# Kernel optimization log

Hardware: AMD Instinct MI355X
Metric: run time of the kernel (lower is better)

Reference implementation:

```python
import math
import jax, jax.numpy as jnp
import numpy as np

VOCAB, EMB, H, NL = 100, 128, 384, 4
B, L = 32, 1024
CTX_IN = 3 * 100


def _glorot(key, shape):
    fan = shape[-1]
    return jax.random.normal(key, shape, dtype=jnp.float32) / np.sqrt(fan)


def setup_inputs() -> dict:
    key = jax.random.key(0)
    ks = jax.random.split(key, 16)
    x = jax.random.randint(ks[0], (B, L), 0, VOCAB)
    context = jax.random.normal(ks[1], (B, L, 3, 100), dtype=jnp.float32)
    h = jnp.zeros((NL, B, H), dtype=jnp.float32)
    c = jnp.zeros((NL, B, H), dtype=jnp.float32)
    emb = _glorot(ks[2], (VOCAB, EMB)).at[71].set(0.0)  # padding_idx=71
    ctx_W = _glorot(ks[3], (EMB, CTX_IN))
    ctx_b = jnp.zeros((EMB,), jnp.float32)
    Wih0 = _glorot(ks[4], (4 * H, 2 * EMB))            # layer 0 input = emb||ctx
    Wih_rest = _glorot(ks[5], (NL - 1, 4 * H, H))
    Whh = _glorot(ks[6], (NL, 4 * H, H))
    bih = jnp.zeros((NL, 4 * H), jnp.float32)
    bhh = jnp.zeros((NL, 4 * H), jnp.float32)
    Wa = _glorot(ks[7], (H, H))
    comb_W = _glorot(ks[8], (H, 2 * H))
    comb_b = jnp.zeros((H,), jnp.float32)
    fc_W = _glorot(ks[9], (VOCAB, H))
    fc_b = jnp.zeros((VOCAB,), jnp.float32)
    return dict(x=x, context=context, h=h, c=c, emb=emb, ctx_W=ctx_W, ctx_b=ctx_b,
                Wih0=Wih0, Wih_rest=Wih_rest, Whh=Whh, bih=bih, bhh=bhh,
                Wa=Wa, comb_W=comb_W, comb_b=comb_b, fc_W=fc_W, fc_b=fc_b)


def _lstm_layer(x, h0, c0, Wih, Whh, bih, bhh):
    # x: [B,L,D] -> scan over time
    def step(carry, xt):
        h, c = carry
        g = xt @ Wih.T + h @ Whh.T + bih + bhh  # [B,4H]
        i, f, gg, o = jnp.split(g, 4, axis=-1)  # torch gate order i,f,g,o
        c = jax.nn.sigmoid(f) * c + jax.nn.sigmoid(i) * jnp.tanh(gg)
        h = jax.nn.sigmoid(o) * jnp.tanh(c)
        return (h, c), h
    (hf, cf), ys = jax.lax.scan(step, (h0, c0), jnp.swapaxes(x, 0, 1))
    return jnp.swapaxes(ys, 0, 1), hf, cf


def _forward(x, context, h, c, emb, ctx_W, ctx_b, Wih0, Wih_rest, Whh, bih, bhh,
             Wa, comb_W, comb_b, fc_W, fc_b):
    x_embed = emb[x]                                        # [B,L,EMB]
    ctx_flat = context.reshape(context.shape[0], context.shape[1], -1)
    ctx_proj = ctx_flat @ ctx_W.T + ctx_b                   # [B,L,EMB]
    inp = jnp.concatenate([x_embed, ctx_proj], axis=-1)     # [B,L,2*EMB]
    hs, cs = [], []
    for l in range(NL):
        Wih = Wih0 if l == 0 else Wih_rest[l - 1]
        inp, hf, cf = _lstm_layer(inp, h[l], c[l], Wih, Whh[l], bih[l], bhh[l])
        hs.append(hf); cs.append(cf)
    out = inp                                               # [B,L,H]
    keys = out @ Wa.T
    scores = jnp.einsum('bqd,bkd->bqk', out, keys) / math.sqrt(H)
    Lq = out.shape[1]
    mask = jnp.tril(jnp.ones((Lq, Lq), dtype=bool))
    scores = jnp.where(mask[None], scores, jnp.float32(-1e30))
    attn = jax.nn.softmax(scores, axis=-1)
    ctx_vec = jnp.einsum('bqk,bkd->bqd', attn, out)
    combined = jnp.tanh(jnp.concatenate([out, ctx_vec], axis=-1) @ comb_W.T + comb_b)
    logits = combined @ fc_W.T + fc_b
    return logits, jnp.stack(hs), jnp.stack(cs)


def reference(x, context, h, c, emb, ctx_W, ctx_b, Wih0, Wih_rest, Whh, bih, bhh,
              Wa, comb_W, comb_b, fc_W, fc_b):
    return _forward(x, context, h, c, emb, ctx_W, ctx_b, Wih0, Wih_rest, Whh,
                    bih, bhh, Wa, comb_W, comb_b, fc_W, fc_b)
```

## Files before the change

kernel.cpp:

```cpp
#include <hip/hip_runtime.h>

typedef unsigned int  uint32;
typedef unsigned long long u64;
typedef unsigned short bf16u;
typedef __attribute__((ext_vector_type(8))) short s8v;
typedef __attribute__((ext_vector_type(4))) float f4v;
typedef __attribute__((ext_vector_type(16))) float f16v;

#define PL   6144
#define PL64 3072
#define PAR  12288
#define HB2  24576

__device__ __forceinline__ float fast_tanh(float x) {
    x = fminf(9.f, fmaxf(-9.f, x));
    float e = __expf(2.f * x);
    return (e - 1.f) / (e + 1.f);
}
__device__ __forceinline__ float sigmoidf(float x) {
    return 1.f / (1.f + __expf(-x));
}
__device__ __forceinline__ bf16u f2bf(float f) {
    uint32 u = __float_as_uint(f);
    u += 0x7fffu + ((u >> 16) & 1u);
    return (bf16u)(u >> 16);
}
__device__ __forceinline__ float bf2f(bf16u u) {
    return __uint_as_float(((uint32)u) << 16);
}
__device__ __forceinline__ uint32 pack2bf(float lo, float hi) {
    return (uint32)f2bf(lo) | ((uint32)f2bf(hi) << 16);
}
__device__ __forceinline__ float bflo(uint32 p) { return __uint_as_float(p << 16); }
__device__ __forceinline__ float bfhi(uint32 p) { return __uint_as_float(p & 0xffff0000u); }

__device__ __forceinline__ s8v ldfrag(const u64* p) {
    union { u64 q[2]; s8v v; } u;
    u.q[0] = __hip_atomic_load(p,     __ATOMIC_RELAXED, __HIP_MEMORY_SCOPE_AGENT);
    u.q[1] = __hip_atomic_load(p + 1, __ATOMIC_RELAXED, __HIP_MEMORY_SCOPE_AGENT);
    return u.v;
}

__global__ void __launch_bounds__(128) embed_ctx_kernel(
    const int* __restrict__ x, const float* __restrict__ ctx,
    const float* __restrict__ emb, const float* __restrict__ ctxW,
    const float* __restrict__ ctxb, bf16u* __restrict__ inp)
{
    const int r0 = blockIdx.x * 16;
    const int tid = threadIdx.x;
    __shared__ float cs[16][301];
    __shared__ int xs[16];
    for (int i = tid; i < 16 * 300; i += 128) {
        int row = i / 300, k = i - row * 300;
        int rt = r0 + row, b = rt & 31, t = rt >> 5;
        cs[row][k] = ctx[((size_t)b * 1024 + t) * 300 + k];
    }
    if (tid < 16) {
        int rt = r0 + tid;
        xs[tid] = x[(rt & 31) * 1024 + (rt >> 5)];
    }
    __syncthreads();
    float acc[16];
    #pragma unroll
    for (int row = 0; row < 16; ++row) acc[row] = 0.f;
    for (int k = 0; k < 300; ++k) {
        float w = ctxW[tid * 300 + k];
        #pragma unroll
        for (int row = 0; row < 16; ++row) acc[row] = fmaf(w, cs[row][k], acc[row]);
    }
    float bb = ctxb[tid];
    for (int row = 0; row < 16; ++row) {
        size_t base = (size_t)(r0 + row) * 256;
        inp[base + tid]       = f2bf(emb[xs[row] * 128 + tid]);
        inp[base + 128 + tid] = f2bf(acc[row] + bb);
    }
}

__global__ void __launch_bounds__(256) gemm_kernel(
    const bf16u* __restrict__ A0, const bf16u* __restrict__ A1, int K0,
    const float* __restrict__ W, const float* __restrict__ bias1,
    void* __restrict__ Cout, int M, int N, int K, int mode)
{
    __shared__ bf16u As[128][40];
    __shared__ bf16u Whi[64][40];
    __shared__ bf16u Wlo[64][40];
    const int tid = threadIdx.x;
    const int bn = blockIdx.x * 64, bm = blockIdx.y * 128;
    const int wave = tid >> 6, lane = tid & 63;
    const int ncol = lane & 15, quad = lane >> 4;
    const int lr = tid >> 2, lk = (tid & 3) * 8;

    f4v acc[2][4];
    #pragma unroll
    for (int i = 0; i < 2; ++i)
        #pragma unroll
        for (int j = 0; j < 4; ++j) acc[i][j] = (f4v){0.f, 0.f, 0.f, 0.f};

    const int wrow = bn + lr;
    for (int k0 = 0; k0 < K; k0 += 32) {
        const bf16u* Ab; int kb, lda;
        if (k0 < K0) { Ab = A0; kb = k0; lda = K0; }
        else         { Ab = A1; kb = k0 - K0; lda = K - K0; }
        uint4 av0 = *(const uint4*)(Ab + (size_t)(bm + lr) * lda + kb + lk);
        uint4 av1 = *(const uint4*)(Ab + (size_t)(bm + 64 + lr) * lda + kb + lk);
        float4 w0 = make_float4(0.f, 0.f, 0.f, 0.f), w1 = w0;
        if (wrow < N) {
            const float* wp = W + (size_t)wrow * K + k0 + lk;
            w0 = *(const float4*)wp;
            w1 = *(const float4*)(wp + 4);
        }
        __syncthreads();
        *(uint4*)&As[lr][lk] = av0;
        *(uint4*)&As[64 + lr][lk] = av1;
        {
            bf16u h[8], l[8];
            float wf[8] = {w0.x, w0.y, w0.z, w0.w, w1.x, w1.y, w1.z, w1.w};
            #pragma unroll
            for (int j = 0; j < 8; ++j) {
                h[j] = f2bf(wf[j]);
                l[j] = f2bf(wf[j] - bf2f(h[j]));
            }
            #pragma unroll
            for (int j = 0; j < 8; ++j) Whi[lr][lk + j] = h[j];
            #pragma unroll
            for (int j = 0; j < 8; ++j) Wlo[lr][lk + j] = l[j];
        }
        __syncthreads();
        s8v aF[2], bH[4], bL[4];
        #pragma unroll
        for (int mt = 0; mt < 2; ++mt)
            aF[mt] = *(const s8v*)&As[wave * 32 + mt * 16 + ncol][quad * 8];
        #pragma unroll
        for (int nt = 0; nt < 4; ++nt) {
            bH[nt] = *(const s8v*)&Whi[nt * 16 + ncol][quad * 8];
            bL[nt] = *(const s8v*)&Wlo[nt * 16 + ncol][quad * 8];
        }
        #pragma unroll
        for (int mt = 0; mt < 2; ++mt)
            #pragma unroll
            for (int nt = 0; nt < 4; ++nt) {
                acc[mt][nt] = __builtin_amdgcn_mfma_f32_16x16x32_bf16(
                    aF[mt], bH[nt], acc[mt][nt], 0, 0, 0);
                acc[mt][nt] = __builtin_amdgcn_mfma_f32_16x16x32_bf16(
                    aF[mt], bL[nt], acc[mt][nt], 0, 0, 0);
            }
    }

    #pragma unroll
    for (int nt = 0; nt < 4; ++nt) {
        const int col = bn + nt * 16 + ncol;
        if (col >= N) continue;
        float bb = bias1 ? bias1[col] : 0.f;
        #pragma unroll
        for (int mt = 0; mt < 2; ++mt) {
            const int rowb = bm + wave * 32 + mt * 16 + quad * 4;
            if (mode == 3) {
                #pragma unroll
                for (int r = 0; r < 4; ++r) {
                    int row = rowb + r;
                    int b = row & 31, t = row >> 5;
                    ((float*)Cout)[((size_t)b * 1024 + t) * (size_t)N + col] =
                        acc[mt][nt][r] + bb;
                }
            } else {
                #pragma unroll
                for (int r = 0; r < 4; ++r) {
                    float v = acc[mt][nt][r] + bb;
                    if (mode == 2) v = fast_tanh(v);
                    ((bf16u*)Cout)[(size_t)(rowb + r) * N + col] = f2bf(v);
                }
            }
        }
    }
}

__device__ __forceinline__ void scoped_barrier(uint32* flags, uint32 r,
                                               int tid, int l, int bid) {
    __syncthreads();
    if (tid == 0)
        __hip_atomic_store(&flags[bid * 32], r, __ATOMIC_RELAXED, __HIP_MEMORY_SCOPE_AGENT);
    const int lo = (l > 0) ? (l - 1) * 48 : 0;
    const int nf = ((l > 0) + 1 + (l < 3)) * 48;
    if (tid < nf) {
        while (__hip_atomic_load(&flags[(lo + tid) * 32], __ATOMIC_RELAXED,
                                 __HIP_MEMORY_SCOPE_AGENT) < r)
            __builtin_amdgcn_s_sleep(1);
    }
    __syncthreads();
}

__global__ void __launch_bounds__(256, 1) lstm_wave_kernel(
    const bf16u* __restrict__ inp,
    const float* __restrict__ Wih0,
    const float* __restrict__ WihR,
    const float* __restrict__ Whh,
    const float* __restrict__ bih, const float* __restrict__ bhh,
    const float* __restrict__ h_in, const float* __restrict__ c_in,
    uint32* __restrict__ y3bm,
    uint32* __restrict__ hbuf,
    uint32* __restrict__ flags,
    float* __restrict__ hs_out, float* __restrict__ cs_out)
{
    extern __shared__ char sm[];
    const int tid = threadIdx.x, bid = blockIdx.x;
    const int l = bid / 48, sub = bid - l * 48;
    const int j0 = sub * 8;
    const int wave = tid >> 6, lane = tid & 63;
    const int row32 = lane & 31;
    const int khalf = lane >> 5;
    const int n = row32;

    const int Kx = l ? 384 : 256;
    const int WSTR = l ? 392 : 264;
    const int wbytes = 2 * 32 * WSTR * 2;
    bf16u* wlds  = (bf16u*)sm;
    float* gates = (float*)(sm + wbytes);

    const float* WhhL = Whh + (size_t)l * 1536 * 384;
    const float* WihL = l ? (WihR + (size_t)(l - 1) * 1536 * 384) : Wih0;
    const float* bihL = bih + l * 1536;
    const float* bhhL = bhh + l * 1536;
    uint32* hbL = hbuf + (size_t)l * HB2;
    uint32* ybL = l ? (hbuf + (size_t)(l - 1) * HB2) : nullptr;

    const int h0c = wave * 6;
    const int x0c = wave * 4;

    s8v Bh6[6], Bl6[6];
    {
        const int wrow = (n >> 3) * 384 + j0 + (n & 7);
        #pragma unroll
        for (int i = 0; i < 6; ++i) {
            const float* wp = WhhL + (size_t)wrow * 384 + (h0c + i) * 16 + khalf * 8;
            s8v hi, lo;
            #pragma unroll
            for (int j = 0; j < 8; ++j) {
                float w = wp[j];
                bf16u wh = f2bf(w);
                bf16u wl = f2bf(w - bf2f(wh));
                hi[j] = (short)wh; lo[j] = (short)wl;
            }
            Bh6[i] = hi; Bl6[i] = lo;
        }
    }
    for (int r2 = 0; r2 < 32; ++r2) {
        int rg = (r2 >> 3) * 384 + j0 + (r2 & 7);
        for (int k = tid; k < Kx; k += 256) {
            float w = WihL[(size_t)rg * Kx + k];
            bf16u wh = f2bf(w);
            wlds[r2 * WSTR + k] = wh;
            wlds[32 * WSTR + r2 * WSTR + k] = f2bf(w - bf2f(wh));
        }
    }

    const int ub = tid & 31, jp = tid >> 5;
    const int jg0 = j0 + 2 * jp;
    const int wbase = (sub * 32 + ub) * 4 + jp;
    float c0r = 0.f, c1r = 0.f, h0l = 0.f, h1l = 0.f;
    float bI0 = 0, bF0 = 0, bG0 = 0, bO0 = 0, bI1 = 0, bF1 = 0, bG1 = 0, bO1 = 0;

    if (tid < 128) {
        bI0 = bihL[jg0] + bhhL[jg0];
        bF0 = bihL[384 + jg0] + bhhL[384 + jg0];
        bG0 = bihL[768 + jg0] + bhhL[768 + jg0];
        bO0 = bihL[1152 + jg0] + bhhL[1152 + jg0];
        bI1 = bihL[jg0 + 1] + bhhL[jg0 + 1];
        bF1 = bihL[384 + jg0 + 1] + bhhL[384 + jg0 + 1];
        bG1 = bihL[768 + jg0 + 1] + bhhL[768 + jg0 + 1];
        bO1 = bihL[1152 + jg0 + 1] + bhhL[1152 + jg0 + 1];
        float ha = h_in[(size_t)l * 12288 + ub * 384 + jg0];
        float hb = h_in[(size_t)l * 12288 + ub * 384 + jg0 + 1];
        bf16u ha_h = f2bf(ha); bf16u ha_l = f2bf(ha - bf2f(ha_h));
        bf16u hb_h = f2bf(hb); bf16u hb_l = f2bf(hb - bf2f(hb_h));
        __hip_atomic_store(&hbL[wbase],
                           (uint32)ha_h | ((uint32)hb_h << 16),
                           __ATOMIC_RELAXED, __HIP_MEMORY_SCOPE_AGENT);
        __hip_atomic_store(&hbL[PL + wbase],
                           (uint32)ha_l | ((uint32)hb_l << 16),
                           __ATOMIC_RELAXED, __HIP_MEMORY_SCOPE_AGENT);
        c0r = c_in[(size_t)l * 12288 + ub * 384 + jg0];
        c1r = c_in[(size_t)l * 12288 + ub * 384 + jg0 + 1];
    }
    scoped_barrier(flags, 1u, tid, l, bid);

    for (int r = 0; r < 1027; ++r) {
        const int t = r - l;
        if ((unsigned)t < 1024u) {
            const u64* hB = (const u64*)(hbL + (t & 1) * PAR);
            uint32* hW = hbL + ((t + 1) & 1) * PAR;

            f16v cHH = {0.f,0.f,0.f,0.f,0.f,0.f,0.f,0.f,
                        0.f,0.f,0.f,0.f,0.f,0.f,0.f,0.f};
            f16v cLH = cHH, cHL = cHH;

            s8v Ah[6], Al[6];
            #pragma unroll
            for (int i = 0; i < 6; ++i) {
                const int co = (((h0c + i) * 2 + khalf) * 32 + row32) * 2;
                Ah[i] = ldfrag(hB + co);
                Al[i] = ldfrag(hB + PL64 + co);
            }

            if (l) {
                const u64* yB = (const u64*)(ybL + ((t + 1) & 1) * PAR);
                s8v Ayh[6], Ayl[6];
                #pragma unroll
                for (int i = 0; i < 6; ++i) {
                    const int co = (((h0c + i) * 2 + khalf) * 32 + row32) * 2;
                    Ayh[i] = ldfrag(yB + co);
                    Ayl[i] = ldfrag(yB + PL64 + co);
                }
                #pragma unroll
                for (int i = 0; i < 6; ++i) {
                    cHH = __builtin_amdgcn_mfma_f32_32x32x16_bf16(Ah[i], Bh6[i], cHH, 0, 0, 0);
                    cLH = __builtin_amdgcn_mfma_f32_32x32x16_bf16(Al[i], Bh6[i], cLH, 0, 0, 0);
                    cHL = __builtin_amdgcn_mfma_f32_32x32x16_bf16(Ah[i], Bl6[i], cHL, 0, 0, 0);
                }
                #pragma unroll
                for (int i = 0; i < 6; ++i) {
                    const int kt = h0c + i;
                    s8v Bxh = *(const s8v*)&wlds[n * 392 + kt * 16 + khalf * 8];
                    s8v Bxl = *(const s8v*)&wlds[32 * 392 + n * 392 + kt * 16 + khalf * 8];
                    cHH = __builtin_amdgcn_mfma_f32_32x32x16_bf16(Ayh[i], Bxh, cHH, 0, 0, 0);
                    cLH = __builtin_amdgcn_mfma_f32_32x32x16_bf16(Ayl[i], Bxh, cLH, 0, 0, 0);
                    cHL = __builtin_amdgcn_mfma_f32_32x32x16_bf16(Ayh[i], Bxl, cHL, 0, 0, 0);
                }
            } else {
                const uint4* irow = (const uint4*)(inp + ((size_t)t * 32 + row32) * 256);
                s8v Ai[4];
                #pragma unroll
                for (int i = 0; i < 4; ++i) {
                    union { uint4 u; s8v v; } cv;
                    cv.u = irow[(x0c + i) * 2 + khalf];
                    Ai[i] = cv.v;
                }
                #pragma unroll
                for (int i = 0; i < 6; ++i) {
                    cHH = __builtin_amdgcn_mfma_f32_32x32x16_bf16(Ah[i], Bh6[i], cHH, 0, 0, 0);
                    cLH = __builtin_amdgcn_mfma_f32_32x32x16_bf16(Al[i], Bh6[i], cLH, 0, 0, 0);
                    cHL = __builtin_amdgcn_mfma_f32_32x32x16_bf16(Ah[i], Bl6[i], cHL, 0, 0, 0);
                }
                #pragma unroll
                for (int i = 0; i < 4; ++i) {
                    const int kt = x0c + i;
                    s8v Bxh = *(const s8v*)&wlds[n * 264 + kt * 16 + khalf * 8];
                    s8v Bxl = *(const s8v*)&wlds[32 * 264 + n * 264 + kt * 16 + khalf * 8];
                    cHH = __builtin_amdgcn_mfma_f32_32x32x16_bf16(Ai[i], Bxh, cHH, 0, 0, 0);
                    cHL = __builtin_amdgcn_mfma_f32_32x32x16_bf16(Ai[i], Bxl, cHL, 0, 0, 0);
                }
            }
            {
                float* ps = gates + wave * 1056;
                #pragma unroll
                for (int reg = 0; reg < 16; ++reg) {
                    const int brow = (reg & 3) + 8 * (reg >> 2) + 4 * khalf;
                    ps[n * 33 + brow] = cHH[reg] + cLH[reg] + cHL[reg];
                }
            }
            __syncthreads();

            if (tid < 128) {
                const int jj0 = 2 * jp, jj1 = 2 * jp + 1;
                #define GS(g) (gates[(g) * 33 + ub] + gates[1056 + (g) * 33 + ub] + \
                               gates[2112 + (g) * 33 + ub] + gates[3168 + (g) * 33 + ub])
                float pi0 = GS(jj0)      + bI0;
                float pf0 = GS(8 + jj0)  + bF0;
                float pg0 = GS(16 + jj0) + bG0;
                float po0 = GS(24 + jj0) + bO0;
                float pi1 = GS(jj1)      + bI1;
                float pf1 = GS(8 + jj1)  + bF1;
                float pg1 = GS(16 + jj1) + bG1;
                float po1 = GS(24 + jj1) + bO1;
                #undef GS
                c0r = sigmoidf(pf0) * c0r + sigmoidf(pi0) * fast_tanh(pg0);
                c1r = sigmoidf(pf1) * c1r + sigmoidf(pi1) * fast_tanh(pg1);
                float hv0 = sigmoidf(po0) * fast_tanh(c0r);
                float hv1 = sigmoidf(po1) * fast_tanh(c1r);
                h0l = hv0; h1l = hv1;
                bf16u h0h = f2bf(hv0); bf16u h0lo = f2bf(hv0 - bf2f(h0h));
                bf16u h1h = f2bf(hv1); bf16u h1lo = f2bf(hv1 - bf2f(h1h));
                uint32 hiw = (uint32)h0h | ((uint32)h1h << 16);
                uint32 low = (uint32)h0lo | ((uint32)h1lo << 16);
                __hip_atomic_store(&hW[wbase], hiw,
                                   __ATOMIC_RELAXED, __HIP_MEMORY_SCOPE_AGENT);
                __hip_atomic_store(&hW[PL + wbase], low,
                                   __ATOMIC_RELAXED, __HIP_MEMORY_SCOPE_AGENT);
                if (l == 3)
                    y3bm[(size_t)t * 6144 + wbase] = hiw;
            }
        }
        scoped_barrier(flags, (uint32)(r + 2), tid, l, bid);
    }

    if (tid < 128) {
        hs_out[(size_t)l * 12288 + ub * 384 + jg0]     = h0l;
        hs_out[(size_t)l * 12288 + ub * 384 + jg0 + 1] = h1l;
        cs_out[(size_t)l * 12288 + ub * 384 + jg0]     = c0r;
        cs_out[(size_t)l * 12288 + ub * 384 + jg0 + 1] = c1r;
    }
}

__global__ void __launch_bounds__(256) transpose_y_kernel(
    const uint32* __restrict__ in, uint32* __restrict__ out)
{
    const int t = blockIdx.x;
    const int tid = threadIdx.x;
    __shared__ uint32 lds[32 * 197];
    const uint32* src = in + (size_t)t * 6144;
    #pragma unroll
    for (int k = 0; k < 24; ++k) {
        int i = k * 256 + tid;
        int sub = i >> 7, b = (i >> 2) & 31, q = i & 3;
        lds[b * 197 + sub * 4 + q] = src[i];
    }
    __syncthreads();
    uint32* dst = out + (size_t)t * 32 * 192;
    #pragma unroll
    for (int k = 0; k < 24; ++k) {
        int i = k * 256 + tid;
        int b = i / 192, c = i - b * 192;
        dst[b * 192 + c] = lds[b * 197 + c];
    }
}

__global__ void __launch_bounds__(256, 1) attn_kernel(
    const bf16u* __restrict__ outy, const bf16u* __restrict__ keys,
    bf16u* __restrict__ ctxv)
{
    extern __shared__ char smem[];
    uint32* Qs  = (uint32*)smem;
    uint32* Ks  = (uint32*)(smem + 26112);
    bf16u*  Vt  = (bf16u*)(smem + 52224);
    float*  Ss  = (float*)(smem + 95232);
    bf16u*  Ph  = (bf16u*)(smem + 112128);
    bf16u*  Pl  = (bf16u*)(smem + 115200);
    float*  m_s = (float*)(smem + 118272);
    float*  l_s = m_s + 32;
    float*  al_s = m_s + 64;

    const int b = blockIdx.y;
    const int q0 = blockIdx.x * 32;
    const int tid = threadIdx.x;
    const int wave = tid >> 6, lane = tid & 63;
    const int lrow = lane & 31, lhalf = lane >> 5;

    for (int i = tid; i < 32 * 192; i += 256) {
        int q = i / 192, dp = i - q * 192;
        Qs[q * 204 + dp] = ((const uint32*)outy)[((size_t)(q0 + q) * 32 + b) * 192 + dp];
    }
    if (tid < 32) { m_s[tid] = -3e38f; l_s[tid] = 0.f; }

    f16v O[3];
    #pragma unroll
    for (int g = 0; g < 3; ++g)
        #pragma unroll
        for (int r = 0; r < 16; ++r) O[g][r] = 0.f;

    const int nkt = blockIdx.x + 1;
    for (int kt = 0; kt < nkt; ++kt) {
        const int k0 = kt * 32;
        __syncthreads();
        for (int i = tid; i < 32 * 192; i += 256) {
            int kk = i / 192, dp = i - kk * 192;
            size_t rb = ((size_t)(k0 + kk) * 32 + b) * 192;
            Ks[kk * 204 + dp] = ((const uint32*)keys)[rb + dp];
            uint32 vv = ((const uint32*)outy)[rb + dp];
            Vt[(2 * dp) * 56 + kk]     = (bf16u)(vv & 0xffffu);
            Vt[(2 * dp + 1) * 56 + kk] = (bf16u)(vv >> 16);
        }
        __syncthreads();

        {
            f16v s;
            #pragma unroll
            for (int r = 0; r < 16; ++r) s[r] = 0.f;
            #pragma unroll
            for (int i6 = 0; i6 < 6; ++i6) {
                const int kc = wave * 6 + i6;
                s8v a  = *(const s8v*)((const bf16u*)Qs + lrow * 408 + kc * 16 + lhalf * 8);
                s8v kb = *(const s8v*)((const bf16u*)Ks + lrow * 408 + kc * 16 + lhalf * 8);
                s = __builtin_amdgcn_mfma_f32_32x32x16_bf16(a, kb, s, 0, 0, 0);
            }
            float* ps = Ss + wave * 1056;
            #pragma unroll
            for (int r = 0; r < 16; ++r) {
                const int q = (r & 3) + 8 * (r >> 2) + 4 * lhalf;
                ps[q * 33 + lrow] = s[r];
            }
        }
        __syncthreads();

        if (tid < 32) {
            const int q = tid;
            float sv[32];
            float mt = m_s[q];
            #pragma unroll
            for (int k = 0; k < 32; ++k) {
                float s = Ss[q * 33 + k] + Ss[1056 + q * 33 + k]
                        + Ss[2112 + q * 33 + k] + Ss[3168 + q * 33 + k];
                s *= 0.051031036307982884f;
                sv[k] = ((k0 + k) <= (q0 + q)) ? s : -1e30f;
                mt = fmaxf(mt, sv[k]);
            }
            float alpha = __expf(m_s[q] - mt);
            float l = l_s[q] * alpha;
            #pragma unroll
            for (int k = 0; k < 32; ++k) {
                float pv = __expf(sv[k] - mt);
                l += pv;
                bf16u ph = f2bf(pv);
                Ph[q * 48 + k] = ph;
                Pl[q * 48 + k] = f2bf(pv - bf2f(ph));
            }
            m_s[q] = mt; l_s[q] = l; al_s[q] = alpha;
        }
        __syncthreads();

        {
            float ar[16];
            #pragma unroll
            for (int r = 0; r < 16; ++r)
                ar[r] = al_s[(r & 3) + 8 * (r >> 2) + 4 * lhalf];
            #pragma unroll
            for (int g = 0; g < 3; ++g)
                #pragma unroll
                for (int r = 0; r < 16; ++r) O[g][r] *= ar[r];

            s8v pa0 = *(const s8v*)(Ph + lrow * 48 + lhalf * 8);
            s8v pa1 = *(const s8v*)(Ph + lrow * 48 + 16 + lhalf * 8);
            s8v pl0 = *(const s8v*)(Pl + lrow * 48 + lhalf * 8);
            s8v pl1 = *(const s8v*)(Pl + lrow * 48 + 16 + lhalf * 8);
            #pragma unroll
            for (int g = 0; g < 3; ++g) {
                const int d = (wave * 3 + g) * 32 + lrow;
                s8v v0 = *(const s8v*)(Vt + d * 56 + lhalf * 8);
                s8v v1 = *(const s8v*)(Vt + d * 56 + 16 + lhalf * 8);
                O[g] = __builtin_amdgcn_mfma_f32_32x32x16_bf16(pa0, v0, O[g], 0, 0, 0);
                O[g] = __builtin_amdgcn_mfma_f32_32x32x16_bf16(pl0, v0, O[g], 0, 0, 0);
                O[g] = __builtin_amdgcn_mfma_f32_32x32x16_bf16(pa1, v1, O[g], 0, 0, 0);
                O[g] = __builtin_amdgcn_mfma_f32_32x32x16_bf16(pl1, v1, O[g], 0, 0, 0);
            }
        }
    }

    __syncthreads();
    if (tid < 32) al_s[tid] = 1.f / l_s[tid];
    __syncthreads();
    {
        float ir[16];
        #pragma unroll
        for (int r = 0; r < 16; ++r)
            ir[r] = al_s[(r & 3) + 8 * (r >> 2) + 4 * lhalf];
        bf16u* Os = (bf16u*)Ks;
        #pragma unroll
        for (int g = 0; g < 3; ++g) {
            const int d = (wave * 3 + g) * 32 + lrow;
            #pragma unroll
            for (int r = 0; r < 16; ++r) {
                const int q = (r & 3) + 8 * (r >> 2) + 4 * lhalf;
                Os[q * 408 + d] = f2bf(O[g][r] * ir[r]);
            }
        }
    }
    __syncthreads();
    for (int i = tid; i < 32 * 192; i += 256) {
        int q = i / 192, dp = i - q * 192;
        ((uint32*)ctxv)[((size_t)(q0 + q) * 32 + b) * 192 + dp] = Ks[q * 204 + dp];
    }
}

extern "C" void kernel_launch(void* const* d_in, const int* in_sizes, int n_in,
                              void* d_out, int out_size, void* d_ws, size_t ws_size,
                              hipStream_t stream) {
    (void)in_sizes; (void)n_in; (void)out_size; (void)ws_size;
    const int*   x        = (const int*)d_in[0];
    const float* context  = (const float*)d_in[1];
    const float* h_in     = (const float*)d_in[2];
    const float* c_in     = (const float*)d_in[3];
    const float* emb      = (const float*)d_in[4];
    const float* ctx_W    = (const float*)d_in[5];
    const float* ctx_b    = (const float*)d_in[6];
    const float* Wih0     = (const float*)d_in[7];
    const float* Wih_rest = (const float*)d_in[8];
    const float* Whh      = (const float*)d_in[9];
    const float* bih      = (const float*)d_in[10];
    const float* bhh      = (const float*)d_in[11];
    const float* Wa       = (const float*)d_in[12];
    const float* comb_W   = (const float*)d_in[13];
    const float* comb_b   = (const float*)d_in[14];
    const float* fc_W     = (const float*)d_in[15];
    const float* fc_b     = (const float*)d_in[16];
    float* out = (float*)d_out;

    char* wsb = (char*)d_ws;
    uint32* flags = (uint32*)(wsb + 0);
    uint32* hbuf  = (uint32*)(wsb + 32768);
    uint32* y3bm  = (uint32*)(wsb + 458752);
    bf16u*  y3    = (bf16u*)(wsb + 25624576ull);
    bf16u*  inp   = (bf16u*)(wsb + 50790400ull);
    bf16u*  keysu = (bf16u*)(wsb + 50790400ull);
    bf16u*  ctxvu = (bf16u*)(wsb + 458752);
    bf16u*  combu = (bf16u*)(wsb + 50790400ull);

    hipMemsetAsync(d_ws, 0, 32768, stream);

    static int smem_set = 0;
    if (!smem_set) {
        hipFuncSetAttribute((const void*)lstm_wave_kernel,
                            hipFuncAttributeMaxDynamicSharedMemorySize, 67072);
        hipFuncSetAttribute((const void*)attn_kernel,
                            hipFuncAttributeMaxDynamicSharedMemorySize, 118656);
        smem_set = 1;
    }

    embed_ctx_kernel<<<2048, 128, 0, stream>>>(x, context, emb, ctx_W, ctx_b, inp);

    const size_t HS_OFF = (size_t)32768 * 100;
    lstm_wave_kernel<<<192, 256, 67072, stream>>>(
        inp, Wih0, Wih_rest, Whh, bih, bhh, h_in, c_in,
        y3bm, hbuf, flags, out + HS_OFF, out + HS_OFF + 49152);

    transpose_y_kernel<<<1024, 256, 0, stream>>>(y3bm, (uint32*)y3);

    gemm_kernel<<<dim3(6, 256), 256, 0, stream>>>(
        y3, nullptr, 384, Wa, nullptr, keysu, 32768, 384, 384, 1);
    attn_kernel<<<dim3(32, 32), 256, 118656, stream>>>(y3, keysu, ctxvu);
    gemm_kernel<<<dim3(6, 256), 256, 0, stream>>>(
        y3, ctxvu, 384, comb_W, comb_b, combu, 32768, 384, 768, 2);
    gemm_kernel<<<dim3(2, 256), 256, 0, stream>>>(
        combu, nullptr, 384, fc_W, fc_b, out, 32768, 100, 384, 3);
}
```

Measured before the change: 5.766 ms.

## Halve LSTM wavefront block count by giving each block 16 hidden units

The persistent LSTM kernel now runs 24 blocks per layer (96 total) instead of 48, and each block computes 16 hidden units with two 32-column MFMA tiles. The hidden-state buffer layout, the scoped barrier fan-in, the LDS weight and gate sizes, and the transpose kernel's indexing all change to match. The aim is to cut the per-step cross-block barrier cost (fewer flags to poll, fewer participants) and reuse the A fragments across two B tiles. In exchange each block does twice the MFMA work per step and needs about 134 KB of LDS.

```diff
diff --git a/kernel.cpp b/kernel.cpp
--- a/kernel.cpp
+++ b/kernel.cpp
@@ -179,8 +179,8 @@
     __syncthreads();
     if (tid == 0)
         __hip_atomic_store(&flags[bid * 32], r, __ATOMIC_RELAXED, __HIP_MEMORY_SCOPE_AGENT);
-    const int lo = (l > 0) ? (l - 1) * 48 : 0;
-    const int nf = ((l > 0) + 1 + (l < 3)) * 48;
+    const int lo = (l > 0) ? (l - 1) * 24 : 0;
+    const int nf = ((l > 0) + 1 + (l < 3)) * 24;
     if (tid < nf) {
         while (__hip_atomic_load(&flags[(lo + tid) * 32], __ATOMIC_RELAXED,
                                  __HIP_MEMORY_SCOPE_AGENT) < r)
@@ -203,16 +203,15 @@
 {
     extern __shared__ char sm[];
     const int tid = threadIdx.x, bid = blockIdx.x;
-    const int l = bid / 48, sub = bid - l * 48;
-    const int j0 = sub * 8;
+    const int l = bid / 24, sub = bid - l * 24;
+    const int j0 = sub * 16;
     const int wave = tid >> 6, lane = tid & 63;
     const int row32 = lane & 31;
     const int khalf = lane >> 5;
-    const int n = row32;
 
     const int Kx = l ? 384 : 256;
     const int WSTR = l ? 392 : 264;
-    const int wbytes = 2 * 32 * WSTR * 2;
+    const int wbytes = 2 * 64 * WSTR * 2;
     bf16u* wlds  = (bf16u*)sm;
     float* gates = (float*)(sm + wbytes);
 
@@ -226,9 +225,11 @@
     const int h0c = wave * 6;
     const int x0c = wave * 4;
 
-    s8v Bh6[6], Bl6[6];
-    {
-        const int wrow = (n >> 3) * 384 + j0 + (n & 7);
+    s8v Bh[2][6], Bl[2][6];
+    #pragma unroll
+    for (int nt = 0; nt < 2; ++nt) {
+        const int n = nt * 32 + row32;
+        const int wrow = (n >> 4) * 384 + j0 + (n & 15);
         #pragma unroll
         for (int i = 0; i < 6; ++i) {
             const float* wp = WhhL + (size_t)wrow * 384 + (h0c + i) * 16 + khalf * 8;
@@ -240,34 +241,33 @@
                 bf16u wl = f2bf(w - bf2f(wh));
                 hi[j] = (short)wh; lo[j] = (short)wl;
             }
-            Bh6[i] = hi; Bl6[i] = lo;
-        }
-    }
-    for (int r2 = 0; r2 < 32; ++r2) {
-        int rg = (r2 >> 3) * 384 + j0 + (r2 & 7);
+            Bh[nt][i] = hi; Bl[nt][i] = lo;
+        }
+    }
+    for (int r2 = 0; r2 < 64; ++r2) {
+        int rg = (r2 >> 4) * 384 + j0 + (r2 & 15);
         for (int k = tid; k < Kx; k += 256) {
             float w = WihL[(size_t)rg * Kx + k];
             bf16u wh = f2bf(w);
             wlds[r2 * WSTR + k] = wh;
-            wlds[32 * WSTR + r2 * WSTR + k] = f2bf(w - bf2f(wh));
+            wlds[64 * WSTR + r2 * WSTR + k] = f2bf(w - bf2f(wh));
         }
     }
 
     const int ub = tid & 31, jp = tid >> 5;
     const int jg0 = j0 + 2 * jp;
-    const int wbase = (sub * 32 + ub) * 4 + jp;
+    const int wbase = (sub * 32 + ub) * 8 + jp;
     float c0r = 0.f, c1r = 0.f, h0l = 0.f, h1l = 0.f;
-    float bI0 = 0, bF0 = 0, bG0 = 0, bO0 = 0, bI1 = 0, bF1 = 0, bG1 = 0, bO1 = 0;
-
-    if (tid < 128) {
-        bI0 = bihL[jg0] + bhhL[jg0];
-        bF0 = bihL[384 + jg0] + bhhL[384 + jg0];
-        bG0 = bihL[768 + jg0] + bhhL[768 + jg0];
-        bO0 = bihL[1152 + jg0] + bhhL[1152 + jg0];
-        bI1 = bihL[jg0 + 1] + bhhL[jg0 + 1];
-        bF1 = bihL[384 + jg0 + 1] + bhhL[384 + jg0 + 1];
-        bG1 = bihL[768 + jg0 + 1] + bhhL[768 + jg0 + 1];
-        bO1 = bihL[1152 + jg0 + 1] + bhhL[1152 + jg0 + 1];
+
+    float bI0 = bihL[jg0] + bhhL[jg0];
+    float bF0 = bihL[384 + jg0] + bhhL[384 + jg0];
+    float bG0 = bihL[768 + jg0] + bhhL[768 + jg0];
+    float bO0 = bihL[1152 + jg0] + bhhL[1152 + jg0];
+    float bI1 = bihL[jg0 + 1] + bhhL[jg0 + 1];
+    float bF1 = bihL[384 + jg0 + 1] + bhhL[384 + jg0 + 1];
+    float bG1 = bihL[768 + jg0 + 1] + bhhL[768 + jg0 + 1];
+    float bO1 = bihL[1152 + jg0 + 1] + bhhL[1152 + jg0 + 1];
+    {
         float ha = h_in[(size_t)l * 12288 + ub * 384 + jg0];
         float hb = h_in[(size_t)l * 12288 + ub * 384 + jg0 + 1];
         bf16u ha_h = f2bf(ha); bf16u ha_l = f2bf(ha - bf2f(ha_h));
@@ -289,14 +289,15 @@
             const u64* hB = (const u64*)(hbL + (t & 1) * PAR);
             uint32* hW = hbL + ((t + 1) & 1) * PAR;
 
-            f16v cHH = {0.f,0.f,0.f,0.f,0.f,0.f,0.f,0.f,
-                        0.f,0.f,0.f,0.f,0.f,0.f,0.f,0.f};
-            f16v cLH = cHH, cHL = cHH;
+            f16v c0HH = {0.f,0.f,0.f,0.f,0.f,0.f,0.f,0.f,
+                         0.f,0.f,0.f,0.f,0.f,0.f,0.f,0.f};
+            f16v c0LH = c0HH, c0HL = c0HH;
+            f16v c1HH = c0HH, c1LH = c0HH, c1HL = c0HH;
 
             s8v Ah[6], Al[6];
             #pragma unroll
             for (int i = 0; i < 6; ++i) {
-                const int co = (((h0c + i) * 2 + khalf) * 32 + row32) * 2;
+                const int co = ((h0c + i) * 32 + row32) * 4 + khalf * 2;
                 Ah[i] = ldfrag(hB + co);
                 Al[i] = ldfrag(hB + PL64 + co);
             }
@@ -306,24 +307,32 @@
                 s8v Ayh[6], Ayl[6];
                 #pragma unroll
                 for (int i = 0; i < 6; ++i) {
-                    const int co = (((h0c + i) * 2 + khalf) * 32 + row32) * 2;
+                    const int co = ((h0c + i) * 32 + row32) * 4 + khalf * 2;
                     Ayh[i] = ldfrag(yB + co);
                     Ayl[i] = ldfrag(yB + PL64 + co);
                 }
                 #pragma unroll
                 for (int i = 0; i < 6; ++i) {
-                    cHH = __builtin_amdgcn_mfma_f32_32x32x16_bf16(Ah[i], Bh6[i], cHH, 0, 0, 0);
-                    cLH = __builtin_amdgcn_mfma_f32_32x32x16_bf16(Al[i], Bh6[i], cLH, 0, 0, 0);
-                    cHL = __builtin_amdgcn_mfma_f32_32x32x16_bf16(Ah[i], Bl6[i], cHL, 0, 0, 0);
+                    c0HH = __builtin_amdgcn_mfma_f32_32x32x16_bf16(Ah[i], Bh[0][i], c0HH, 0, 0, 0);
+                    c0LH = __builtin_amdgcn_mfma_f32_32x32x16_bf16(Al[i], Bh[0][i], c0LH, 0, 0, 0);
+                    c0HL = __builtin_amdgcn_mfma_f32_32x32x16_bf16(Ah[i], Bl[0][i], c0HL, 0, 0, 0);
+                    c1HH = __builtin_amdgcn_mfma_f32_32x32x16_bf16(Ah[i], Bh[1][i], c1HH, 0, 0, 0);
+                    c1LH = __builtin_amdgcn_mfma_f32_32x32x16_bf16(Al[i], Bh[1][i], c1LH, 0, 0, 0);
+                    c1HL = __builtin_amdgcn_mfma_f32_32x32x16_bf16(Ah[i], Bl[1][i], c1HL, 0, 0, 0);
                 }
                 #pragma unroll
                 for (int i = 0; i < 6; ++i) {
                     const int kt = h0c + i;
-                    s8v Bxh = *(const s8v*)&wlds[n * 392 + kt * 16 + khalf * 8];
-                    s8v Bxl = *(const s8v*)&wlds[32 * 392 + n * 392 + kt * 16 + khalf * 8];
-                    cHH = __builtin_amdgcn_mfma_f32_32x32x16_bf16(Ayh[i], Bxh, cHH, 0, 0, 0);
-                    cLH = __builtin_amdgcn_mfma_f32_32x32x16_bf16(Ayl[i], Bxh, cLH, 0, 0, 0);
-                    cHL = __builtin_amdgcn_mfma_f32_32x32x16_bf16(Ayh[i], Bxl, cHL, 0, 0, 0);
+                    s8v B0h = *(const s8v*)&wlds[row32 * 392 + kt * 16 + khalf * 8];
+                    s8v B0l = *(const s8v*)&wlds[64 * 392 + row32 * 392 + kt * 16 + khalf * 8];
+                    s8v B1h = *(const s8v*)&wlds[(32 + row32) * 392 + kt * 16 + khalf * 8];
+                    s8v B1l = *(const s8v*)&wlds[64 * 392 + (32 + row32) * 392 + kt * 16 + khalf * 8];
+                    c0HH = __builtin_amdgcn_mfma_f32_32x32x16_bf16(Ayh[i], B0h, c0HH, 0, 0, 0);
+                    c0LH = __builtin_amdgcn_mfma_f32_32x32x16_bf16(Ayl[i], B0h, c0LH, 0, 0, 0);
+                    c0HL = __builtin_amdgcn_mfma_f32_32x32x16_bf16(Ayh[i], B0l, c0HL, 0, 0, 0);
+                    c1HH = __builtin_amdgcn_mfma_f32_32x32x16_bf16(Ayh[i], B1h, c1HH, 0, 0, 0);
+                    c1LH = __builtin_amdgcn_mfma_f32_32x32x16_bf16(Ayl[i], B1h, c1LH, 0, 0, 0);
+                    c1HL = __builtin_amdgcn_mfma_f32_32x32x16_bf16(Ayh[i], B1l, c1HL, 0, 0, 0);
                 }
             } else {
                 const uint4* irow = (const uint4*)(inp + ((size_t)t * 32 + row32) * 256);
@@ -336,41 +345,49 @@
                 }
                 #pragma unroll
                 for (int i = 0; i < 6; ++i) {
-                    cHH = __builtin_amdgcn_mfma_f32_32x32x16_bf16(Ah[i], Bh6[i], cHH, 0, 0, 0);
-                    cLH = __builtin_amdgcn_mfma_f32_32x32x16_bf16(Al[i], Bh6[i], cLH, 0, 0, 0);
-                    cHL = __builtin_amdgcn_mfma_f32_32x32x16_bf16(Ah[i], Bl6[i], cHL, 0, 0, 0);
+                    c0HH = __builtin_amdgcn_mfma_f32_32x32x16_bf16(Ah[i], Bh[0][i], c0HH, 0, 0, 0);
+                    c0LH = __builtin_amdgcn_mfma_f32_32x32x16_bf16(Al[i], Bh[0][i], c0LH, 0, 0, 0);
+                    c0HL = __builtin_amdgcn_mfma_f32_32x32x16_bf16(Ah[i], Bl[0][i], c0HL, 0, 0, 0);
+                    c1HH = __builtin_amdgcn_mfma_f32_32x32x16_bf16(Ah[i], Bh[1][i], c1HH, 0, 0, 0);
+                    c1LH = __builtin_amdgcn_mfma_f32_32x32x16_bf16(Al[i], Bh[1][i], c1LH, 0, 0, 0);
+                    c1HL = __builtin_amdgcn_mfma_f32_32x32x16_bf16(Ah[i], Bl[1][i], c1HL, 0, 0, 0);
                 }
                 #pragma unroll
                 for (int i = 0; i < 4; ++i) {
                     const int kt = x0c + i;
-                    s8v Bxh = *(const s8v*)&wlds[n * 264 + kt * 16 + khalf * 8];
-                    s8v Bxl = *(const s8v*)&wlds[32 * 264 + n * 264 + kt * 16 + khalf * 8];
-                    cHH = __builtin_amdgcn_mfma_f32_32x32x16_bf16(Ai[i], Bxh, cHH, 0, 0, 0);
-                    cHL = __builtin_amdgcn_mfma_f32_32x32x16_bf16(Ai[i], Bxl, cHL, 0, 0, 0);
+                    s8v B0h = *(const s8v*)&wlds[row32 * 264 + kt * 16 + khalf * 8];
+                    s8v B0l = *(const s8v*)&wlds[64 * 264 + row32 * 264 + kt * 16 + khalf * 8];
+                    s8v B1h = *(const s8v*)&wlds[(32 + row32) * 264 + kt * 16 + khalf * 8];
+                    s8v B1l = *(const s8v*)&wlds[64 * 264 + (32 + row32) * 264 + kt * 16 + khalf * 8];
+                    c0HH = __builtin_amdgcn_mfma_f32_32x32x16_bf16(Ai[i], B0h, c0HH, 0, 0, 0);
+                    c0HL = __builtin_amdgcn_mfma_f32_32x32x16_bf16(Ai[i], B0l, c0HL, 0, 0, 0);
+                    c1HH = __builtin_amdgcn_mfma_f32_32x32x16_bf16(Ai[i], B1h, c1HH, 0, 0, 0);
+                    c1HL = __builtin_amdgcn_mfma_f32_32x32x16_bf16(Ai[i], B1l, c1HL, 0, 0, 0);
                 }
             }
             {
-                float* ps = gates + wave * 1056;
+                float* ps = gates + wave * 2112;
                 #pragma unroll
                 for (int reg = 0; reg < 16; ++reg) {
                     const int brow = (reg & 3) + 8 * (reg >> 2) + 4 * khalf;
-                    ps[n * 33 + brow] = cHH[reg] + cLH[reg] + cHL[reg];
+                    ps[row32 * 33 + brow] = c0HH[reg] + c0LH[reg] + c0HL[reg];
+                    ps[(32 + row32) * 33 + brow] = c1HH[reg] + c1LH[reg] + c1HL[reg];
                 }
             }
             __syncthreads();
 
-            if (tid < 128) {
+            {
                 const int jj0 = 2 * jp, jj1 = 2 * jp + 1;
-                #define GS(g) (gates[(g) * 33 + ub] + gates[1056 + (g) * 33 + ub] + \
-                               gates[2112 + (g) * 33 + ub] + gates[3168 + (g) * 33 + ub])
+                #define GS(g) (gates[(g) * 33 + ub] + gates[2112 + (g) * 33 + ub] + \
+                               gates[4224 + (g) * 33 + ub] + gates[6336 + (g) * 33 + ub])
                 float pi0 = GS(jj0)      + bI0;
-                float pf0 = GS(8 + jj0)  + bF0;
-                float pg0 = GS(16 + jj0) + bG0;
-                float po0 = GS(24 + jj0) + bO0;
+                float pf0 = GS(16 + jj0) + bF0;
+                float pg0 = GS(32 + jj0) + bG0;
+                float po0 = GS(48 + jj0) + bO0;
                 float pi1 = GS(jj1)      + bI1;
-                float pf1 = GS(8 + jj1)  + bF1;
-                float pg1 = GS(16 + jj1) + bG1;
-                float po1 = GS(24 + jj1) + bO1;
+                float pf1 = GS(16 + jj1) + bF1;
+                float pg1 = GS(32 + jj1) + bG1;
+                float po1 = GS(48 + jj1) + bO1;
                 #undef GS
                 c0r = sigmoidf(pf0) * c0r + sigmoidf(pi0) * fast_tanh(pg0);
                 c1r = sigmoidf(pf1) * c1r + sigmoidf(pi1) * fast_tanh(pg1);
@@ -392,7 +409,7 @@
         scoped_barrier(flags, (uint32)(r + 2), tid, l, bid);
     }
 
-    if (tid < 128) {
+    {
         hs_out[(size_t)l * 12288 + ub * 384 + jg0]     = h0l;
         hs_out[(size_t)l * 12288 + ub * 384 + jg0 + 1] = h1l;
         cs_out[(size_t)l * 12288 + ub * 384 + jg0]     = c0r;
@@ -410,8 +427,8 @@
     #pragma unroll
     for (int k = 0; k < 24; ++k) {
         int i = k * 256 + tid;
-        int sub = i >> 7, b = (i >> 2) & 31, q = i & 3;
-        lds[b * 197 + sub * 4 + q] = src[i];
+        int sub = i >> 8, b = (i >> 3) & 31, q = i & 7;
+        lds[b * 197 + sub * 8 + q] = src[i];
     }
     __syncthreads();
     uint32* dst = out + (size_t)t * 32 * 192;
@@ -607,7 +624,7 @@
     static int smem_set = 0;
     if (!smem_set) {
         hipFuncSetAttribute((const void*)lstm_wave_kernel,
-                            hipFuncAttributeMaxDynamicSharedMemorySize, 67072);
+                            hipFuncAttributeMaxDynamicSharedMemorySize, 134144);
         hipFuncSetAttribute((const void*)attn_kernel,
                             hipFuncAttributeMaxDynamicSharedMemorySize, 118656);
         smem_set = 1;
@@ -616,7 +633,7 @@
     embed_ctx_kernel<<<2048, 128, 0, stream>>>(x, context, emb, ctx_W, ctx_b, inp);
 
     const size_t HS_OFF = (size_t)32768 * 100;
-    lstm_wave_kernel<<<192, 256, 67072, stream>>>(
+    lstm_wave_kernel<<<96, 256, 134144, stream>>>(
         inp, Wih0, Wih_rest, Whh, bih, bhh, h_in, c_in,
         y3bm, hbuf, flags, out + HS_OFF, out + HS_OFF + 49152);
 
```

Result: slower. 6.511 ms (+12.9%).
